# Optimization experiments

Measured on AMD Instinct MI355X. Metric: run time of the kernel, lower is better.

Reference implementation:

```python
import jax, jax.numpy as jnp
import numpy as np

EMBED = 1024
HEADS = 16
HEAD_DIM = EMBED // HEADS


def setup_inputs() -> dict:
    key = jax.random.key(0)
    ks = jax.random.split(key, 8)
    N, S = 4, 2048
    values = jax.random.normal(ks[0], (N, S, EMBED), dtype=jnp.float32)
    keys = jax.random.normal(ks[1], (N, S, EMBED), dtype=jnp.float32)
    query = jax.random.normal(ks[2], (N, S, EMBED), dtype=jnp.float32)
    mask = jnp.ones((N, 1, 1, S), dtype=jnp.int32)
    sd = 1.0 / np.sqrt(HEAD_DIM)
    Wv = jax.random.uniform(ks[3], (HEAD_DIM, HEAD_DIM), jnp.float32, -sd, sd)
    Wk = jax.random.uniform(ks[4], (HEAD_DIM, HEAD_DIM), jnp.float32, -sd, sd)
    Wq = jax.random.uniform(ks[5], (HEAD_DIM, HEAD_DIM), jnp.float32, -sd, sd)
    so = 1.0 / np.sqrt(EMBED)
    Wo = jax.random.uniform(ks[6], (EMBED, EMBED), jnp.float32, -so, so)
    bo = jax.random.uniform(ks[7], (EMBED,), jnp.float32, -so, so)
    return {"values": values, "keys": keys, "query": query, "mask": mask,
            "Wv": Wv, "Wk": Wk, "Wq": Wq, "Wo": Wo, "bo": bo}


def reference(values, keys, query, mask, Wv, Wk, Wq, Wo, bo):
    N, Sq, _ = query.shape
    # split heads: (N, L, H, D)
    v = values.reshape(N, -1, HEADS, HEAD_DIM)
    k = keys.reshape(N, -1, HEADS, HEAD_DIM)
    q = query.reshape(N, Sq, HEADS, HEAD_DIM)
    # per-head linear projections (torch Linear: x @ W.T)
    v = jnp.einsum('nlhd,ed->nlhe', v, Wv)
    k = jnp.einsum('nlhd,ed->nlhe', k, Wk)
    q = jnp.einsum('nqhd,ed->nqhe', q, Wq)
    # energy: (N, H, Q, K)
    energy = jnp.einsum('nqhd,nkhd->nhqk', q, k)
    energy = jnp.where(mask == 0, jnp.float32(-1e20), energy)
    # NOTE: original scales by sqrt(embed_size), not sqrt(head_dim)
    attention = jax.nn.softmax(energy / jnp.sqrt(jnp.float32(EMBED)), axis=3)
    out = jnp.einsum('nhql,nlhd->nqhd', attention, v).reshape(N, Sq, EMBED)
    return out @ Wo.T + bo
```

## Files before the change

kernel.cpp:

```cpp
#include <hip/hip_runtime.h>
#include <hip/hip_bf16.h>

typedef __bf16 bf16x8 __attribute__((ext_vector_type(8)));
typedef __bf16 bf16x4 __attribute__((ext_vector_type(4)));
typedef __bf16 bf16x2 __attribute__((ext_vector_type(2)));
typedef float  f32x4  __attribute__((ext_vector_type(4)));
typedef float  f32x16 __attribute__((ext_vector_type(16)));
typedef unsigned int u32;
typedef u32 u32x4 __attribute__((ext_vector_type(4)));

#define S_  2048
#define E_  1024
#define NH_ 64

__device__ __forceinline__ f32x4 mfma16(bf16x8 a, bf16x8 b, f32x4 c) {
    return __builtin_amdgcn_mfma_f32_16x16x32_bf16(a, b, c, 0, 0, 0);
}
__device__ __forceinline__ f32x16 mfma32(bf16x8 a, bf16x8 b, f32x16 c) {
    return __builtin_amdgcn_mfma_f32_32x32x16_bf16(a, b, c, 0, 0, 0);
}
__device__ __forceinline__ u32 pack2(float a, float b) {
    bf16x2 t; t[0] = (__bf16)a; t[1] = (__bf16)b;
    return __builtin_bit_cast(u32, t);
}
__device__ __forceinline__ void swap32(u32& a, u32& b) {
    asm("v_permlane32_swap_b32 %0, %1" : "+v"(a), "+v"(b));
}
__device__ __forceinline__ f32x16 zero16() {
    f32x16 z;
#pragma unroll
    for (int i = 0; i < 16; ++i) z[i] = 0.f;
    return z;
}
__device__ __forceinline__ void gload_lds16(const void* g, void* l) {
    __builtin_amdgcn_global_load_lds(
        (const __attribute__((address_space(1))) unsigned int*)g,
        (__attribute__((address_space(3))) unsigned int*)l, 16, 0, 0);
}
__device__ __forceinline__ bf16x8 lds_frag(const char* p0, const char* p1) {
    bf16x4 lo = *(const bf16x4*)p0;
    bf16x4 hi = *(const bf16x4*)p1;
    bf16x8 f;
    f[0] = lo[0]; f[1] = lo[1]; f[2] = lo[2]; f[3] = lo[3];
    f[4] = hi[0]; f[5] = hi[1]; f[6] = hi[2]; f[7] = hi[3];
    return f;
}

__global__ __launch_bounds__(256) void k_cast_wo(const float* __restrict__ Wo,
                                                 __bf16* __restrict__ Wob) {
    int i = (blockIdx.x * 256 + threadIdx.x) * 8;
    int o = i >> 10, e0 = i & 1023;
    float4 a = *(const float4*)(Wo + i);
    float4 b = *(const float4*)(Wo + i + 4);
    bf16x8 f;
    f[0] = (__bf16)a.x; f[1] = (__bf16)a.y; f[2] = (__bf16)a.z; f[3] = (__bf16)a.w;
    f[4] = (__bf16)b.x; f[5] = (__bf16)b.y; f[6] = (__bf16)b.z; f[7] = (__bf16)b.w;
    int e_swz = (e0 & ~63) | ((e0 & 63) ^ ((o & 7) << 3));
    *(bf16x8*)(Wob + (size_t)o * 1024 + e_swz) = f;
}

__global__ __launch_bounds__(256) void k_proj(const float* __restrict__ vin,
                                              const float* __restrict__ kin,
                                              const float* __restrict__ qin,
                                              const float* __restrict__ Wv,
                                              const float* __restrict__ Wk,
                                              const float* __restrict__ Wq,
                                              __bf16* __restrict__ Qws,
                                              __bf16* __restrict__ Kws,
                                              __bf16* __restrict__ Vt) {
    const int z = blockIdx.z;
    const float* in = (z == 0) ? vin : ((z == 1) ? kin : qin);
    const float* W  = (z == 0) ? Wv  : ((z == 1) ? Wk  : Wq);
    const float scale = (z == 2) ? 0.04508422f : 1.0f;
    const int bid  = blockIdx.x;
    const int nh   = bid >> 5;
    const int sblk = (bid & 31) << 6;
    const int n = nh >> 4, h = nh & 15;
    const int lane = threadIdx.x & 63, wid = threadIdx.x >> 6;
    const int l16 = lane & 15, g = lane >> 4;

    bf16x8 Bf[4][2];
#pragma unroll
    for (int nt = 0; nt < 4; ++nt)
#pragma unroll
        for (int ks = 0; ks < 2; ++ks) {
            const float* wp = W + (nt * 16 + l16) * 64 + ks * 32 + g * 8;
            float4 a = *(const float4*)wp;
            float4 b = *(const float4*)(wp + 4);
            bf16x8 f;
            f[0] = (__bf16)(a.x * scale); f[1] = (__bf16)(a.y * scale);
            f[2] = (__bf16)(a.z * scale); f[3] = (__bf16)(a.w * scale);
            f[4] = (__bf16)(b.x * scale); f[5] = (__bf16)(b.y * scale);
            f[6] = (__bf16)(b.z * scale); f[7] = (__bf16)(b.w * scale);
            Bf[nt][ks] = f;
        }

    const int s = sblk + wid * 16 + l16;
    const float* ip = in + ((size_t)n * S_ + s) * E_ + h * 64 + g * 8;
    bf16x8 Af[2];
#pragma unroll
    for (int ks = 0; ks < 2; ++ks) {
        float4 a = *(const float4*)(ip + ks * 32);
        float4 b = *(const float4*)(ip + ks * 32 + 4);
        bf16x8 f;
        f[0] = (__bf16)a.x; f[1] = (__bf16)a.y; f[2] = (__bf16)a.z; f[3] = (__bf16)a.w;
        f[4] = (__bf16)b.x; f[5] = (__bf16)b.y; f[6] = (__bf16)b.z; f[7] = (__bf16)b.w;
        Af[ks] = f;
    }

    f32x4 acc[4];
#pragma unroll
    for (int nt = 0; nt < 4; ++nt) { acc[nt][0] = 0.f; acc[nt][1] = 0.f; acc[nt][2] = 0.f; acc[nt][3] = 0.f; }

    if (z == 0) {
#pragma unroll
        for (int nt = 0; nt < 4; ++nt) {
            acc[nt] = mfma16(Bf[nt][0], Af[0], acc[nt]);
            acc[nt] = mfma16(Bf[nt][1], Af[1], acc[nt]);
        }
#pragma unroll
        for (int nt = 0; nt < 4; ++nt)
#pragma unroll
            for (int r = 0; r < 4; ++r) {
                int e = nt * 16 + g * 4 + r;
                int srow = sblk + wid * 16 + l16;
                int sc = srow ^ (((e & 7) << 3) | (((e >> 3) & 1) << 2));
                Vt[((size_t)nh * 64 + e) * S_ + sc] = (__bf16)acc[nt][r];
            }
    } else {
#pragma unroll
        for (int nt = 0; nt < 4; ++nt) {
            acc[nt] = mfma16(Af[0], Bf[nt][0], acc[nt]);
            acc[nt] = mfma16(Af[1], Bf[nt][1], acc[nt]);
        }
        if (z == 1) {
#pragma unroll
            for (int nt = 0; nt < 4; ++nt)
#pragma unroll
                for (int r = 0; r < 4; ++r) {
                    int srow = sblk + wid * 16 + g * 4 + r;
                    int ec = (nt * 16 + l16) ^ (((srow & 7) << 3) | (((srow >> 3) & 1) << 2));
                    Kws[((size_t)nh * S_ + srow) * 64 + ec] = (__bf16)acc[nt][r];
                }
        } else {
#pragma unroll
            for (int nt = 0; nt < 4; ++nt)
#pragma unroll
                for (int r = 0; r < 4; ++r) {
                    int srow = sblk + wid * 16 + g * 4 + r;
                    Qws[((size_t)nh * S_ + srow) * 64 + nt * 16 + l16] = (__bf16)acc[nt][r];
                }
        }
    }
}

__global__ __launch_bounds__(256, 2) void k_attn(const __bf16* __restrict__ Qws,
                                                 const __bf16* __restrict__ Kws,
                                                 const __bf16* __restrict__ Vt,
                                                 const int* __restrict__ maskp,
                                                 __bf16* __restrict__ Xws) {
    __shared__ __align__(16) char lds[2][16384];
    const int tid = threadIdx.x, lane = tid & 63, wid = tid >> 6;
    const int l31 = lane & 31, hf = lane >> 5, h8 = hf * 8;
    const int v = blockIdx.x;
    const int u = v >> 3;
    const int nh = (v & 7) * 8 + (u & 7), qb = u >> 3;
    const int n = nh >> 4, hd = nh & 15;

    int az = 0;
    for (int i = tid; i < S_; i += 256) az |= (maskp[(size_t)n * S_ + i] == 0);
    const int anyzero = __syncthreads_or(az);

    const char* Kc = (const char*)(Kws + (size_t)nh * S_ * 64);
    const char* Vc = (const char*)(Vt  + (size_t)nh * 64 * S_);
    const __bf16* Qb = Qws + (size_t)nh * S_ * 64;

    const int q0 = qb * 256 + wid * 64;
    bf16x8 QfA[4], QfB[4];
#pragma unroll
    for (int dt = 0; dt < 4; ++dt) {
        QfA[dt] = *(const bf16x8*)(Qb + (size_t)(q0 + l31) * 64 + dt * 16 + h8);
        QfB[dt] = *(const bf16x8*)(Qb + (size_t)(q0 + 32 + l31) * 64 + dt * 16 + h8);
    }

    f32x16 accA0 = zero16(), accA1 = zero16(), accB0 = zero16(), accB1 = zero16();
    float lsumA = 0.f, lsumB = 0.f;

    auto stage = [&](int buf, int kb) {
        char* base = &lds[buf][0];
        const char* ks = Kc + (size_t)kb * 8192 + wid * 2048 + lane * 16;
        char* kd = base + wid * 2048;
        gload_lds16(ks, kd);
        gload_lds16(ks + 1024, kd + 1024);
        const int r0 = wid * 16 + (lane >> 3);
        const char* vs = Vc + (size_t)r0 * (S_ * 2) + (size_t)kb * 128 + (lane & 7) * 16;
        char* vd = base + 8192 + wid * 2048;
        gload_lds16(vs, vd);
        gload_lds16(vs + (size_t)8 * (S_ * 2), vd + 1024);
    };

    const int fs = ((l31 & 7) << 4) | (((l31 >> 3) & 1) << 3);

    auto softmax = [&](const f32x16& s, float& ls, int kbase, bf16x8& P0, bf16x8& P1) {
        f32x16 sv = s;
        if (anyzero) {
#pragma unroll
            for (int r = 0; r < 16; ++r) {
                int kk = kbase + (r & 3) + 8 * (r >> 2) + 4 * hf;
                if (maskp[(size_t)n * S_ + kk] == 0) sv[r] = -1e30f;
            }
        }
        float p[16];
#pragma unroll
        for (int r = 0; r < 16; ++r) p[r] = __builtin_amdgcn_exp2f(sv[r]);
        ls += ((((p[0] + p[1]) + (p[2] + p[3])) + ((p[4] + p[5]) + (p[6] + p[7])))
            + (((p[8] + p[9]) + (p[10] + p[11])) + ((p[12] + p[13]) + (p[14] + p[15]))));
        u32 w0 = pack2(p[0],  p[1]),  w1 = pack2(p[2],  p[3]);
        u32 w2 = pack2(p[4],  p[5]),  w3 = pack2(p[6],  p[7]);
        u32 w4 = pack2(p[8],  p[9]),  w5 = pack2(p[10], p[11]);
        u32 w6 = pack2(p[12], p[13]), w7 = pack2(p[14], p[15]);
        swap32(w0, w2); swap32(w1, w3); swap32(w4, w6); swap32(w5, w7);
        u32x4 t0; t0[0] = w0; t0[1] = w1; t0[2] = w2; t0[3] = w3;
        u32x4 t1; t1[0] = w4; t1[1] = w5; t1[2] = w6; t1[3] = w7;
        P0 = __builtin_bit_cast(bf16x8, t0);
        P1 = __builtin_bit_cast(bf16x8, t1);
    };

    stage(0, 0);
    int buf = 0;
    for (int kb = 0; kb < 32; ++kb) {
        __syncthreads();
        if (kb < 31) stage(buf ^ 1, kb + 1);
        char* base = &lds[buf][0];
        char* vbase = base + 8192;
        const int k0 = kb * 64;
#pragma unroll
        for (int kt = 0; kt < 2; ++kt) {
            const char* krow = base + (kt * 32 + l31) * 128;
            bf16x8 K0 = lds_frag(krow + ((0 * 32 + hf * 16) ^ fs), krow + ((0 * 32 + hf * 16 + 8) ^ fs));
            bf16x8 K1 = lds_frag(krow + ((1 * 32 + hf * 16) ^ fs), krow + ((1 * 32 + hf * 16 + 8) ^ fs));
            bf16x8 K2 = lds_frag(krow + ((2 * 32 + hf * 16) ^ fs), krow + ((2 * 32 + hf * 16 + 8) ^ fs));
            bf16x8 K3 = lds_frag(krow + ((3 * 32 + hf * 16) ^ fs), krow + ((3 * 32 + hf * 16 + 8) ^ fs));
            __builtin_amdgcn_s_setprio(1);
            f32x16 sA = zero16(), sB = zero16();
            sA = mfma32(K0, QfA[0], sA); sA = mfma32(K1, QfA[1], sA);
            sA = mfma32(K2, QfA[2], sA); sA = mfma32(K3, QfA[3], sA);
            sB = mfma32(K0, QfB[0], sB); sB = mfma32(K1, QfB[1], sB);
            sB = mfma32(K2, QfB[2], sB); sB = mfma32(K3, QfB[3], sB);
            __builtin_amdgcn_s_setprio(0);
            const char* v0row = vbase + (0 * 32 + l31) * 128;
            const char* v1row = vbase + (1 * 32 + l31) * 128;
            const int o0b = (kt * 2 + 0) * 32 + hf * 16;
            const int o1b = (kt * 2 + 1) * 32 + hf * 16;
            bf16x8 V00 = lds_frag(v0row + (o0b ^ fs), v0row + ((o0b + 8) ^ fs));
            bf16x8 V01 = lds_frag(v0row + (o1b ^ fs), v0row + ((o1b + 8) ^ fs));
            bf16x8 V10 = lds_frag(v1row + (o0b ^ fs), v1row + ((o0b + 8) ^ fs));
            bf16x8 V11 = lds_frag(v1row + (o1b ^ fs), v1row + ((o1b + 8) ^ fs));
            bf16x8 PA0, PA1, PB0, PB1;
            softmax(sA, lsumA, k0 + kt * 32, PA0, PA1);
            softmax(sB, lsumB, k0 + kt * 32, PB0, PB1);
            __builtin_amdgcn_s_setprio(1);
            accA0 = mfma32(V00, PA0, accA0); accA0 = mfma32(V01, PA1, accA0);
            accA1 = mfma32(V10, PA0, accA1); accA1 = mfma32(V11, PA1, accA1);
            accB0 = mfma32(V00, PB0, accB0); accB0 = mfma32(V01, PB1, accB0);
            accB1 = mfma32(V10, PB0, accB1); accB1 = mfma32(V11, PB1, accB1);
            __builtin_amdgcn_s_setprio(0);
        }
        buf ^= 1;
    }

    lsumA += __shfl_xor(lsumA, 32);
    lsumB += __shfl_xor(lsumB, 32);
    const float invA = 1.0f / lsumA, invB = 1.0f / lsumB;

    auto store_q = [&](const f32x16& a0, const f32x16& a1, int qg, float inv) {
        __bf16* Ob = Xws + ((size_t)(n * S_ + qg)) * E_ + hd * 64;
        const int qsw = (qg & 7) << 3;
#pragma unroll
        for (int dv = 0; dv < 2; ++dv) {
            const f32x16& a = dv ? a1 : a0;
#pragma unroll
            for (int rr = 0; rr < 4; ++rr) {
                bf16x4 o;
#pragma unroll
                for (int j = 0; j < 4; ++j) o[j] = (__bf16)(a[rr * 4 + j] * inv);
                int dsw = ((dv * 32 + rr * 8) ^ qsw) + hf * 4;
                *(bf16x4*)(Ob + dsw) = o;
            }
        }
    };
    store_q(accA0, accA1, q0 + l31, invA);
    store_q(accB0, accB1, q0 + 32 + l31, invB);
}

__global__ __launch_bounds__(256) void k_out(const __bf16* __restrict__ Xws,
                                             const __bf16* __restrict__ Wob,
                                             const float* __restrict__ bo,
                                             float* __restrict__ out) {
    __shared__ __align__(16) char Al[2][16384];
    __shared__ __align__(16) char Bl[2][16384];
    const int tid = threadIdx.x, lane = tid & 63, wid = tid >> 6;
    const int l31 = lane & 31, hf = lane >> 5;
    const int v = blockIdx.x;
    const int id2 = (v & 7) * 64 + (v >> 3);
    const int mb = id2 >> 3, ob = id2 & 7;
    const int m0 = mb * 128, o0 = ob * 128;
    const int wr = wid >> 1, wc = wid & 1;

    const char* Xb = (const char*)Xws + (size_t)m0 * 2048;
    const char* Wb = (const char*)Wob + (size_t)o0 * 2048;
    const int r = tid >> 3, cb = (tid & 7) * 16;

    auto stage = [&](int buf, int kb) {
#pragma unroll
        for (int p = 0; p < 4; ++p) {
            gload_lds16(Xb + (size_t)(p * 32 + r) * 2048 + kb * 128 + cb,
                        &Al[buf][p * 4096 + wid * 1024]);
            gload_lds16(Wb + (size_t)(p * 32 + r) * 2048 + kb * 128 + cb,
                        &Bl[buf][p * 4096 + wid * 1024]);
        }
    };

    f32x16 acc00 = zero16(), acc01 = zero16(), acc10 = zero16(), acc11 = zero16();

    const int arow0 = (wr * 64 + l31) * 128;
    const int brow0 = (wc * 64 + l31) * 128;
    const int rsw = (l31 & 7) << 4;

    stage(0, 0);
    int buf = 0;
    for (int kb = 0; kb < 16; ++kb) {
        __syncthreads();
        if (kb < 15) stage(buf ^ 1, kb + 1);
        const char* ab = &Al[buf][0];
        const char* bb = &Bl[buf][0];
#pragma unroll
        for (int ks = 0; ks < 4; ++ks) {
            const int co = (ks * 32 + hf * 16) ^ rsw;
            bf16x8 A0 = *(const bf16x8*)(ab + arow0 + co);
            bf16x8 A1 = *(const bf16x8*)(ab + arow0 + 32 * 128 + co);
            bf16x8 B0 = *(const bf16x8*)(bb + brow0 + co);
            bf16x8 B1 = *(const bf16x8*)(bb + brow0 + 32 * 128 + co);
            __builtin_amdgcn_s_setprio(1);
            acc00 = mfma32(A0, B0, acc00);
            acc01 = mfma32(A0, B1, acc01);
            acc10 = mfma32(A1, B0, acc10);
            acc11 = mfma32(A1, B1, acc11);
            __builtin_amdgcn_s_setprio(0);
        }
        buf ^= 1;
    }

    const float bias0 = bo[o0 + wc * 64 + l31];
    const float bias1 = bo[o0 + wc * 64 + 32 + l31];
#pragma unroll
    for (int sm = 0; sm < 2; ++sm) {
        const f32x16& a0 = (sm == 0) ? acc00 : acc10;
        const f32x16& a1 = (sm == 0) ? acc01 : acc11;
#pragma unroll
        for (int rr = 0; rr < 4; ++rr)
#pragma unroll
            for (int j = 0; j < 4; ++j) {
                size_t m = (size_t)m0 + wr * 64 + sm * 32 + rr * 8 + hf * 4 + j;
                out[m * E_ + o0 + wc * 64 + l31]      = a0[rr * 4 + j] + bias0;
                out[m * E_ + o0 + wc * 64 + 32 + l31] = a1[rr * 4 + j] + bias1;
            }
    }
}

extern "C" void kernel_launch(void* const* d_in, const int* in_sizes, int n_in,
                              void* d_out, int out_size, void* d_ws, size_t ws_size,
                              hipStream_t stream) {
    const float* vin  = (const float*)d_in[0];
    const float* kin  = (const float*)d_in[1];
    const float* qin  = (const float*)d_in[2];
    const int*   mask = (const int*)d_in[3];
    const float* Wv   = (const float*)d_in[4];
    const float* Wk   = (const float*)d_in[5];
    const float* Wq   = (const float*)d_in[6];
    const float* Wo   = (const float*)d_in[7];
    const float* bo   = (const float*)d_in[8];

    __bf16* Qws = (__bf16*)d_ws;
    __bf16* Kws = Qws + (size_t)NH_ * S_ * 64;
    __bf16* Vt  = Kws + (size_t)NH_ * S_ * 64;
    __bf16* Xws = Vt  + (size_t)NH_ * S_ * 64;
    __bf16* Wob = Xws + (size_t)4 * S_ * E_;
    float* out = (float*)d_out;

    hipLaunchKernelGGL(k_cast_wo, dim3(512), dim3(256), 0, stream, Wo, Wob);
    hipLaunchKernelGGL(k_proj, dim3(2048, 1, 3), dim3(256), 0, stream,
                       vin, kin, qin, Wv, Wk, Wq, Qws, Kws, Vt);
    hipLaunchKernelGGL(k_attn, dim3(512), dim3(256), 0, stream, Qws, Kws, Vt, mask, Xws);
    hipLaunchKernelGGL(k_out, dim3(512), dim3(256), 0, stream, Xws, Wob, bo, out);
}
```

Baseline: 166.8 us.

## Halve attention block size to double grid and vectorize projection stores

The attention kernel now uses 128-thread blocks covering 128 queries each and launches 1024 blocks, with the K/V staging loop rewritten so two waves fill the same 16KB tile. The aim is more blocks per CU and better latency hiding. The cost is that each K/V tile is reused by fewer queries, so K/V traffic doubles. The projection kernel swaps MFMA operand order so each lane writes four contiguous bf16 values as one 8-byte store instead of scattered 2-byte stores, and the LDS fragment loads are simplified via bit casts.

```diff
diff --git a/kernel.cpp b/kernel.cpp
--- a/kernel.cpp
+++ b/kernel.cpp
@@ -7,6 +7,7 @@
 typedef float  f32x4  __attribute__((ext_vector_type(4)));
 typedef float  f32x16 __attribute__((ext_vector_type(16)));
 typedef unsigned int u32;
+typedef u32 u32x2 __attribute__((ext_vector_type(2)));
 typedef u32 u32x4 __attribute__((ext_vector_type(4)));
 
 #define S_  2048
@@ -38,12 +39,10 @@
         (__attribute__((address_space(3))) unsigned int*)l, 16, 0, 0);
 }
 __device__ __forceinline__ bf16x8 lds_frag(const char* p0, const char* p1) {
-    bf16x4 lo = *(const bf16x4*)p0;
-    bf16x4 hi = *(const bf16x4*)p1;
-    bf16x8 f;
-    f[0] = lo[0]; f[1] = lo[1]; f[2] = lo[2]; f[3] = lo[3];
-    f[4] = hi[0]; f[5] = hi[1]; f[6] = hi[2]; f[7] = hi[3];
-    return f;
+    u32x2 lo = *(const u32x2*)p0;
+    u32x2 hi = *(const u32x2*)p1;
+    u32x4 t; t[0] = lo[0]; t[1] = lo[1]; t[2] = hi[0]; t[3] = hi[1];
+    return __builtin_bit_cast(bf16x8, t);
 }
 
 __global__ __launch_bounds__(256) void k_cast_wo(const float* __restrict__ Wo,
@@ -115,46 +114,48 @@
     if (z == 0) {
 #pragma unroll
         for (int nt = 0; nt < 4; ++nt) {
+            acc[nt] = mfma16(Af[0], Bf[nt][0], acc[nt]);
+            acc[nt] = mfma16(Af[1], Bf[nt][1], acc[nt]);
+        }
+#pragma unroll
+        for (int nt = 0; nt < 4; ++nt) {
+            int d = nt * 16 + l16;
+            int s0 = (sblk + wid * 16 + g * 4) ^ (((d & 7) << 3) | (((d >> 3) & 1) << 2));
+            bf16x4 o;
+#pragma unroll
+            for (int r = 0; r < 4; ++r) o[r] = (__bf16)acc[nt][r];
+            *(bf16x4*)(Vt + ((size_t)nh * 64 + d) * S_ + s0) = o;
+        }
+    } else {
+#pragma unroll
+        for (int nt = 0; nt < 4; ++nt) {
             acc[nt] = mfma16(Bf[nt][0], Af[0], acc[nt]);
             acc[nt] = mfma16(Bf[nt][1], Af[1], acc[nt]);
         }
-#pragma unroll
-        for (int nt = 0; nt < 4; ++nt)
-#pragma unroll
-            for (int r = 0; r < 4; ++r) {
-                int e = nt * 16 + g * 4 + r;
-                int srow = sblk + wid * 16 + l16;
-                int sc = srow ^ (((e & 7) << 3) | (((e >> 3) & 1) << 2));
-                Vt[((size_t)nh * 64 + e) * S_ + sc] = (__bf16)acc[nt][r];
+        const int srow = sblk + wid * 16 + l16;
+        if (z == 1) {
+            const int fk = ((srow & 7) << 3) | (((srow >> 3) & 1) << 2);
+#pragma unroll
+            for (int nt = 0; nt < 4; ++nt) {
+                int e0 = (nt * 16 + g * 4) ^ fk;
+                bf16x4 o;
+#pragma unroll
+                for (int r = 0; r < 4; ++r) o[r] = (__bf16)acc[nt][r];
+                *(bf16x4*)(Kws + ((size_t)nh * S_ + srow) * 64 + e0) = o;
             }
-    } else {
-#pragma unroll
-        for (int nt = 0; nt < 4; ++nt) {
-            acc[nt] = mfma16(Af[0], Bf[nt][0], acc[nt]);
-            acc[nt] = mfma16(Af[1], Bf[nt][1], acc[nt]);
-        }
-        if (z == 1) {
-#pragma unroll
-            for (int nt = 0; nt < 4; ++nt)
-#pragma unroll
-                for (int r = 0; r < 4; ++r) {
-                    int srow = sblk + wid * 16 + g * 4 + r;
-                    int ec = (nt * 16 + l16) ^ (((srow & 7) << 3) | (((srow >> 3) & 1) << 2));
-                    Kws[((size_t)nh * S_ + srow) * 64 + ec] = (__bf16)acc[nt][r];
-                }
         } else {
 #pragma unroll
-            for (int nt = 0; nt < 4; ++nt)
-#pragma unroll
-                for (int r = 0; r < 4; ++r) {
-                    int srow = sblk + wid * 16 + g * 4 + r;
-                    Qws[((size_t)nh * S_ + srow) * 64 + nt * 16 + l16] = (__bf16)acc[nt][r];
-                }
-        }
-    }
-}
-
-__global__ __launch_bounds__(256, 2) void k_attn(const __bf16* __restrict__ Qws,
+            for (int nt = 0; nt < 4; ++nt) {
+                bf16x4 o;
+#pragma unroll
+                for (int r = 0; r < 4; ++r) o[r] = (__bf16)acc[nt][r];
+                *(bf16x4*)(Qws + ((size_t)nh * S_ + srow) * 64 + nt * 16 + g * 4) = o;
+            }
+        }
+    }
+}
+
+__global__ __launch_bounds__(128, 2) void k_attn(const __bf16* __restrict__ Qws,
                                                  const __bf16* __restrict__ Kws,
                                                  const __bf16* __restrict__ Vt,
                                                  const int* __restrict__ maskp,
@@ -168,14 +169,14 @@
     const int n = nh >> 4, hd = nh & 15;
 
     int az = 0;
-    for (int i = tid; i < S_; i += 256) az |= (maskp[(size_t)n * S_ + i] == 0);
+    for (int i = tid; i < S_; i += 128) az |= (maskp[(size_t)n * S_ + i] == 0);
     const int anyzero = __syncthreads_or(az);
 
     const char* Kc = (const char*)(Kws + (size_t)nh * S_ * 64);
     const char* Vc = (const char*)(Vt  + (size_t)nh * 64 * S_);
     const __bf16* Qb = Qws + (size_t)nh * S_ * 64;
 
-    const int q0 = qb * 256 + wid * 64;
+    const int q0 = qb * 128 + wid * 64;
     bf16x8 QfA[4], QfB[4];
 #pragma unroll
     for (int dt = 0; dt < 4; ++dt) {
@@ -188,15 +189,19 @@
 
     auto stage = [&](int buf, int kb) {
         char* base = &lds[buf][0];
-        const char* ks = Kc + (size_t)kb * 8192 + wid * 2048 + lane * 16;
-        char* kd = base + wid * 2048;
-        gload_lds16(ks, kd);
-        gload_lds16(ks + 1024, kd + 1024);
-        const int r0 = wid * 16 + (lane >> 3);
-        const char* vs = Vc + (size_t)r0 * (S_ * 2) + (size_t)kb * 128 + (lane & 7) * 16;
-        char* vd = base + 8192 + wid * 2048;
-        gload_lds16(vs, vd);
-        gload_lds16(vs + (size_t)8 * (S_ * 2), vd + 1024);
+        const char* ksrc = Kc + (size_t)kb * 8192;
+#pragma unroll
+        for (int i = 0; i < 4; ++i) {
+            int o = i * 2048 + wid * 1024;
+            gload_lds16(ksrc + o + lane * 16, base + o);
+        }
+        const char* vsrc = Vc + (size_t)kb * 128 + (size_t)(lane >> 3) * (S_ * 2) + (lane & 7) * 16;
+#pragma unroll
+        for (int i = 0; i < 4; ++i) {
+            int o = i * 2048 + wid * 1024;
+            int r0 = o >> 7;
+            gload_lds16(vsrc + (size_t)r0 * (S_ * 2), base + 8192 + o);
+        }
     };
 
     const int fs = ((l31 & 7) << 4) | (((l31 >> 3) & 1) << 3);
@@ -391,6 +396,6 @@
     hipLaunchKernelGGL(k_cast_wo, dim3(512), dim3(256), 0, stream, Wo, Wob);
     hipLaunchKernelGGL(k_proj, dim3(2048, 1, 3), dim3(256), 0, stream,
                        vin, kin, qin, Wv, Wk, Wq, Qws, Kws, Vt);
-    hipLaunchKernelGGL(k_attn, dim3(512), dim3(256), 0, stream, Qws, Kws, Vt, mask, Xws);
+    hipLaunchKernelGGL(k_attn, dim3(1024), dim3(128), 0, stream, Qws, Kws, Vt, mask, Xws);
     hipLaunchKernelGGL(k_out, dim3(512), dim3(256), 0, stream, Xws, Wob, bo, out);
 }
```

Measured after the change: 172.4 us (median of 2 runs). +3.4%, slower.
